# Performance work log

Hardware: AMD Instinct MI355X
Metric: run time of the kernel (lower is better)

The kernel has to match this reference:

```python
import jax, jax.numpy as jnp
import numpy as np
from jax.scipy.special import logsumexp

PAD_IDX, SOS_IDX, EOS_IDX = 0, 1, 2
NEG = -10000.0


def setup_inputs() -> dict:
    B, T, L = 64, 256, 8
    K, E, H = 128, 256, 512      # num_tags, EMBED_SIZE, HIDDEN_SIZE
    CV, WV = 128, 50000          # char / word vocab
    key = jax.random.key(0)
    ks = jax.random.split(key, 12)
    lengths = jax.random.randint(ks[0], (B,), T // 2, T + 1)
    mask = jnp.arange(T)[None, :] < lengths[:, None]          # [B,T] contiguous prefix
    wx = jnp.where(mask, jax.random.randint(ks[1], (B, T), 3, WV), 0).astype(jnp.int32)
    cx = jax.random.randint(ks[2], (B, T, L), 0, CV).astype(jnp.int32)
    y_body = jnp.where(mask, jax.random.randint(ks[3], (B, T), 3, K), PAD_IDX)
    y = jnp.concatenate([jnp.full((B, 1), SOS_IDX, jnp.int32), y_body.astype(jnp.int32)], 1)  # [B,T+1]
    s = 0.05
    char_emb = s * jax.random.normal(ks[4], (CV, E), jnp.float32)
    word_emb = s * jax.random.normal(ks[5], (WV, E), jnp.float32)
    Wi = s * jax.random.normal(ks[6], (E, 4 * H), jnp.float32)
    Wh = s * jax.random.normal(ks[7], (H, 4 * H), jnp.float32)
    b = jnp.zeros((4 * H,), jnp.float32)
    Wout = s * jax.random.normal(ks[8], (H, K), jnp.float32)
    bout = jnp.zeros((K,), jnp.float32)
    trans = jax.random.normal(ks[9], (K, K), jnp.float32)
    trans = trans.at[SOS_IDX, :].set(NEG)
    trans = trans.at[:, EOS_IDX].set(NEG)
    trans = trans.at[:, PAD_IDX].set(NEG)
    trans = trans.at[PAD_IDX, :].set(NEG)
    trans = trans.at[PAD_IDX, EOS_IDX].set(0.0)
    trans = trans.at[PAD_IDX, PAD_IDX].set(0.0)
    return dict(cx=cx, wx=wx, y=y, char_emb=char_emb, word_emb=word_emb,
                Wi=Wi, Wh=Wh, b=b, Wout=Wout, bout=bout, trans=trans)


def _forward(cx, wx, y, char_emb, word_emb, Wi, Wh, b, Wout, bout, trans):
    B, T = wx.shape
    K = trans.shape[0]
    H = Wh.shape[0]
    mask = (wx > 0)                                            # [B,T] bool
    maskf = mask.astype(jnp.float32)
    # embedding: word lookup + mean-pooled char lookup
    x = word_emb[wx] + char_emb[cx].mean(axis=2)               # [B,T,E]

    # masked LSTM (equivalent to pack_padded for prefix masks)
    def lstm_step(carry, inp):
        h, c = carry
        xt, mt = inp                                            # [B,E], [B,1]
        z = xt @ Wi + h @ Wh + b                                # [B,4H]
        i, f, g, o = jnp.split(z, 4, axis=-1)
        i, f, o = jax.nn.sigmoid(i), jax.nn.sigmoid(f), jax.nn.sigmoid(o)
        c_new = f * c + i * jnp.tanh(g)
        h_new = o * jnp.tanh(c_new)
        h = jnp.where(mt, h_new, h)
        c = jnp.where(mt, c_new, c)
        return (h, c), h

    h0 = jnp.zeros((B, H), x.dtype)
    xs = jnp.swapaxes(x, 0, 1)                                  # [T,B,E]
    ms = jnp.swapaxes(mask, 0, 1)[..., None]                    # [T,B,1]
    _, hs = jax.lax.scan(lstm_step, (h0, h0), (xs, ms))         # [T,B,H]
    hs = jnp.swapaxes(hs, 0, 1)                                 # [B,T,H]
    h = (hs @ Wout + bout) * maskf[..., None]                   # emissions [B,T,K]

    # CRF forward algorithm (log partition Z)
    score0 = jnp.full((B, K), NEG, h.dtype).at[:, SOS_IDX].set(0.0)

    def crf_step(score, inp):
        em, mt = inp                                            # [B,K], [B,1]
        s_t = logsumexp(score[:, None, :] + em[:, :, None] + trans[None, :, :], axis=-1)
        return jnp.where(mt, s_t, score), None

    emT = jnp.swapaxes(h, 0, 1)                                 # [T,B,K]
    scoreZ, _ = jax.lax.scan(crf_step, score0, (emT, ms))
    Z = logsumexp(scoreZ + trans[EOS_IDX], axis=-1)             # [B]

    # gold path score
    y_prev, y_next = y[:, :-1], y[:, 1:]                        # [B,T]
    emit = jnp.take_along_axis(h, y_next[..., None], axis=-1)[..., 0]  # [B,T]
    tr = trans[y_next, y_prev]                                  # [B,T]
    gold = jnp.sum((emit + tr) * maskf, axis=1)                 # [B]
    lengths = mask.sum(axis=1)
    last_tag = y[jnp.arange(B), lengths]                        # y has T+1 cols
    gold = gold + trans[EOS_IDX, last_tag]
    return Z - gold                                             # NLL per sequence [B]


def reference(cx, wx, y, char_emb, word_emb, Wi, Wh, b, Wout, bout, trans):
    return _forward(cx, wx, y, char_emb, word_emb, Wi, Wh, b, Wout, bout, trans)
```

## Files before the change

### kernel.cpp

```cpp
#include <hip/hip_runtime.h>


typedef float f32x4 __attribute__((ext_vector_type(4)));
typedef float f32x16 __attribute__((ext_vector_type(16)));
typedef __bf16 bf16x8 __attribute__((ext_vector_type(8)));
typedef unsigned int u32x4 __attribute__((ext_vector_type(4)));
typedef unsigned int u32x2 __attribute__((ext_vector_type(2)));

#define T_LEN 256
#define BB    64
#define EE    256
#define HH    512
#define KK    128
#define KCAT  768

static __device__ inline unsigned f2bf(float f) {
  union { float f; unsigned u; } v; v.f = f;
  unsigned r = v.u + 0x7FFF + ((v.u >> 16) & 1);
  return r >> 16;
}
static __device__ inline float sigm(float x) { return 1.f / (1.f + __expf(-x)); }
static __device__ inline float tanh_fast(float x) {
  return 1.f - 2.f / (1.f + __expf(2.f * x));
}
static __device__ inline bf16x8 ubf(u32x4 v) {
  union { u32x4 u; bf16x8 b; } c; c.u = v; return c.b;
}

__global__ __launch_bounds__(256) void build_wcat(
    const float* __restrict__ Wi, const float* __restrict__ Wh,
    unsigned short* __restrict__ WcatT) {
  __shared__ float tile[64][65];
  int ct = blockIdx.x & 31, kt = blockIdx.x >> 5;
  int tc = threadIdx.x & 63, tr = threadIdx.x >> 6;
  int c0 = ct * 64, k0 = kt * 64;
#pragma unroll
  for (int i = 0; i < 16; ++i) {
    int r = tr * 16 + i, k = k0 + r;
    float v = (k < EE) ? Wi[(size_t)k * 2048 + c0 + tc]
                       : Wh[(size_t)(k - EE) * 2048 + c0 + tc];
    tile[r][tc] = v;
  }
  __syncthreads();
#pragma unroll
  for (int i = 0; i < 16; ++i) {
    int cL = tr * 16 + i;
    WcatT[(size_t)(c0 + cL) * KCAT + k0 + tc] = (unsigned short)f2bf(tile[tc][cL]);
  }
}

__global__ __launch_bounds__(256) void build_wout(
    const float* __restrict__ Wout, unsigned short* __restrict__ WoutT) {
  __shared__ float tile[64][65];
  int ct = blockIdx.x & 1, kt = blockIdx.x >> 1;
  int tc = threadIdx.x & 63, tr = threadIdx.x >> 6;
  int c0 = ct * 64, k0 = kt * 64;
#pragma unroll
  for (int i = 0; i < 16; ++i) {
    int r = tr * 16 + i;
    tile[r][tc] = Wout[(size_t)(k0 + r) * KK + c0 + tc];
  }
  __syncthreads();
#pragma unroll
  for (int i = 0; i < 16; ++i) {
    int cL = tr * 16 + i;
    WoutT[(size_t)(c0 + cL) * HH + k0 + tc] = (unsigned short)f2bf(tile[tc][cL]);
  }
}

__global__ __launch_bounds__(256) void embed_kernel(
    const int* __restrict__ wx, const int* __restrict__ cx,
    const float* __restrict__ we, const float* __restrict__ ce,
    unsigned short* __restrict__ x) {
  int bid = blockIdx.x;
  int t = bid >> 6, b = bid & 63;
  int e = threadIdx.x;
  int w = wx[b * T_LEN + t];
  float v = we[(size_t)w * EE + e];
  const int* cp = cx + ((size_t)(b * T_LEN + t)) * 8;
  float s = 0.f;
#pragma unroll
  for (int l = 0; l < 8; ++l) s += ce[(size_t)cp[l] * EE + e];
  v += s * 0.125f;
  x[(size_t)bid * EE + e] = (unsigned short)f2bf(v);
}

__global__ void zero_flags(unsigned int* __restrict__ f) {
  unsigned z = 0u;
  asm volatile("global_store_dword %0, %1, off sc0 sc1"
               :: "v"(f + threadIdx.x), "v"(z) : "memory");
}

#define SBAR __builtin_amdgcn_sched_barrier(0)
#define WAITV(N) do { asm volatile("s_waitcnt vmcnt(" #N ")" ::: "memory"); SBAR; } while (0)
#define LDC(dst, ptr, OFF) \
  asm volatile("global_load_dwordx4 %0, %1, off offset:" OFF " sc0 sc1" \
               : "=v"(dst) : "v"(ptr) : "memory")
#define LDN(dst, ptr, OFF) \
  asm volatile("global_load_dwordx4 %0, %1, off offset:" OFF \
               : "=v"(dst) : "v"(ptr) : "memory")

#define ISSUE_X(B, P) do { \
  LDN(B[0],P,"0");   LDN(B[1],P,"32");  LDN(B[2],P,"64");  LDN(B[3],P,"96"); \
  LDN(B[4],P,"128"); LDN(B[5],P,"160"); LDN(B[6],P,"192"); LDN(B[7],P,"224"); \
  LDN(B[8],P,"256"); LDN(B[9],P,"288"); LDN(B[10],P,"320"); LDN(B[11],P,"352"); \
  LDN(B[12],P,"384"); LDN(B[13],P,"416"); LDN(B[14],P,"448"); LDN(B[15],P,"480"); } while (0)
#define ISSUE_H0(B, P) do { \
  LDC(B[0],P,"0");   LDC(B[1],P,"32");  LDC(B[2],P,"64");  LDC(B[3],P,"96"); \
  LDC(B[4],P,"128"); LDC(B[5],P,"160"); LDC(B[6],P,"192"); LDC(B[7],P,"224"); \
  LDC(B[8],P,"256"); LDC(B[9],P,"288"); LDC(B[10],P,"320"); LDC(B[11],P,"352"); \
  LDC(B[12],P,"384"); LDC(B[13],P,"416"); LDC(B[14],P,"448"); LDC(B[15],P,"480"); } while (0)
#define ISSUE_H1(B, P) do { \
  LDC(B[0],P,"512"); LDC(B[1],P,"544"); LDC(B[2],P,"576"); LDC(B[3],P,"608"); \
  LDC(B[4],P,"640"); LDC(B[5],P,"672"); LDC(B[6],P,"704"); LDC(B[7],P,"736"); \
  LDC(B[8],P,"768"); LDC(B[9],P,"800"); LDC(B[10],P,"832"); LDC(B[11],P,"864"); \
  LDC(B[12],P,"896"); LDC(B[13],P,"928"); LDC(B[14],P,"960"); LDC(B[15],P,"992"); } while (0)

#define GATES_STORE(T) do { \
    bool mk = ((int)wxv) > 0; \
    _Pragma("unroll") \
    for (int r = 0; r < 4; ++r) { \
      float zi = acc[r], zf = acc[4 + r], zg = acc[8 + r], zo = acc[12 + r]; \
      float cn = sigm(zf) * cst[r] + sigm(zi) * tanh_fast(zg); \
      float hn = sigm(zo) * tanh_fast(cn); \
      if (mk) { cst[r] = cn; hst[r] = hn; } \
    } \
    u32x2 ph; \
    ph[0] = f2bf(hst[0]) | (f2bf(hst[1]) << 16); \
    ph[1] = f2bf(hst[2]) | (f2bf(hst[3]) << 16); \
    asm volatile("global_store_dwordx2 %0, %1, off sc0 sc1" \
                 :: "v"(hstore + (size_t)(T) * 65536), "v"(ph) : "memory"); \
  } while (0)

__global__ __launch_bounds__(128, 1) void lstm_persistent(
    const unsigned short* __restrict__ x,
    unsigned short* __restrict__ hs,
    const unsigned short* __restrict__ WcatT,
    const float* __restrict__ bias,
    const int* __restrict__ wx,
    unsigned int* __restrict__ flags) {
  const int tid = threadIdx.x;
  const int lane = tid & 63;
  const int bhalf = tid >> 6;
  const int hi = lane >> 5;
  const int batch = bhalf * 32 + (lane & 31);
  const int u0 = blockIdx.x * 8;
  const int rr = lane & 31;
  const int wcol = (rr >> 3) * HH + u0 + (rr & 7);

  bf16x8 wreg[48];
#pragma unroll
  for (int kf = 0; kf < 48; ++kf)
    wreg[kf] = *(const bf16x8*)(WcatT + (size_t)wcol * KCAT + kf * 16 + hi * 8);

  float bv[16];
#pragma unroll
  for (int q = 0; q < 4; ++q)
#pragma unroll
    for (int r = 0; r < 4; ++r)
      bv[q * 4 + r] = bias[q * HH + u0 + 4 * hi + r];

  const char* xlane  = (const char*)x  + ((size_t)batch * EE + hi * 8) * 2;
  const char* hread  = (const char*)hs + ((size_t)batch * HH + hi * 8) * 2;
  char*       hstore = (char*)hs + ((size_t)batch * HH + u0 + 4 * hi) * 2;
  const int*  wxp    = wx + batch * T_LEN;

  float cst[4] = {0.f, 0.f, 0.f, 0.f};
  float hst[4] = {0.f, 0.f, 0.f, 0.f};
  u32x4 bufX[16], bufH[16];
  unsigned wxv;
  f32x16 acc;

  ISSUE_X(bufX, xlane);
  asm volatile("global_load_dword %0, %1, off" : "=v"(wxv) : "v"(wxp) : "memory");
  WAITV(0);
#pragma unroll
  for (int i = 0; i < 16; ++i) acc[i] = bv[i];
#pragma unroll
  for (int kf = 0; kf < 16; ++kf)
    acc = __builtin_amdgcn_mfma_f32_32x32x16_bf16(wreg[kf], ubf(bufX[kf]), acc, 0, 0, 0);
  GATES_STORE(0);
  WAITV(0);
  __syncthreads();
  if (tid == 0)
    __hip_atomic_store(flags + blockIdx.x, 1u, __ATOMIC_RELAXED, __HIP_MEMORY_SCOPE_AGENT);

  for (int t = 1; t < T_LEN; ++t) {
    const char* xt = xlane + (size_t)t * 32768;
    const char* hp = hread + (size_t)(t - 1) * 65536;

    ISSUE_X(bufX, xt);
    asm volatile("global_load_dword %0, %1, off" : "=v"(wxv) : "v"(wxp + t) : "memory");
    {
      unsigned v;
      do {
        asm volatile("global_load_dword %0, %1, off sc0 sc1\n\ts_waitcnt vmcnt(0)"
                     : "=v"(v) : "v"(flags + lane) : "memory");
      } while (!__all((int)(v >= (unsigned)t)));
      SBAR;
    }
    ISSUE_H0(bufH, hp);
#pragma unroll
    for (int i = 0; i < 16; ++i) acc[i] = bv[i];
#pragma unroll
    for (int kf = 0; kf < 16; ++kf)
      acc = __builtin_amdgcn_mfma_f32_32x32x16_bf16(wreg[kf], ubf(bufX[kf]), acc, 0, 0, 0);
    SBAR;
    ISSUE_H1(bufX, hp);
    WAITV(16);
#pragma unroll
    for (int kf = 0; kf < 16; ++kf)
      acc = __builtin_amdgcn_mfma_f32_32x32x16_bf16(wreg[16 + kf], ubf(bufH[kf]), acc, 0, 0, 0);
    WAITV(0);
#pragma unroll
    for (int kf = 0; kf < 16; ++kf)
      acc = __builtin_amdgcn_mfma_f32_32x32x16_bf16(wreg[32 + kf], ubf(bufX[kf]), acc, 0, 0, 0);
    GATES_STORE(t);
    WAITV(0);
    __syncthreads();
    if (tid == 0)
      __hip_atomic_store(flags + blockIdx.x, (unsigned)(t + 1),
                         __ATOMIC_RELAXED, __HIP_MEMORY_SCOPE_AGENT);
  }
}

__global__ __launch_bounds__(512) void em_gemm(
    const unsigned short* __restrict__ hs,
    const unsigned short* __restrict__ WoutT,
    const float* __restrict__ bout,
    const int* __restrict__ wx,
    float* __restrict__ em) {
  int mg = blockIdx.x;
  int wave = threadIdx.x >> 6, lane = threadIdx.x & 63;
  int m = wave >> 1, nh = wave & 1;
  int arow = lane & 15, kg = (lane >> 4) * 8;
  int rbase = mg * 64 + m * 16;
  const unsigned short* A = hs + (size_t)(rbase + arow) * HH + kg;
  f32x4 acc[4];
#pragma unroll
  for (int nt = 0; nt < 4; ++nt) acc[nt] = (f32x4){0.f, 0.f, 0.f, 0.f};
#pragma unroll
  for (int ks = 0; ks < 16; ++ks) {
    bf16x8 a = *(const bf16x8*)(A + ks * 32);
#pragma unroll
    for (int nt = 0; nt < 4; ++nt) {
      const unsigned short* Bp =
          WoutT + (size_t)(nh * 64 + nt * 16 + arow) * HH + kg + ks * 32;
      acc[nt] = __builtin_amdgcn_mfma_f32_16x16x32_bf16(a, *(const bf16x8*)Bp, acc[nt], 0, 0, 0);
    }
  }
#pragma unroll
  for (int nt = 0; nt < 4; ++nt) {
    int n = nh * 64 + nt * 16 + arow;
    float bo = bout[n];
#pragma unroll
    for (int r = 0; r < 4; ++r) {
      int row = rbase + (lane >> 4) * 4 + r;
      int t = row >> 6, b = row & 63;
      float v = (acc[nt][r] + bo) * ((wx[b * T_LEN + t] > 0) ? 1.f : 0.f);
      em[(size_t)row * KK + n] = v;
    }
  }
}

__global__ __launch_bounds__(512) void crf_kernel(
    const float* __restrict__ em,
    const float* __restrict__ trans,
    const int* __restrict__ wx,
    const int* __restrict__ y,
    float* __restrict__ out) {
  int b = blockIdx.x;
  __shared__ float tl[KK][129];
  __shared__ float El[KK][129];
  __shared__ float sc[KK];
  __shared__ float p[KK];
  __shared__ float red[512];
  __shared__ float red2[512];
  __shared__ float mshare[2];
  int tid = threadIdx.x;
  for (int i = tid; i < KK * KK; i += 512) {
    float v = trans[i];
    tl[i >> 7][i & 127] = v;
    El[i >> 7][i & 127] = __expf(v);
  }
  if (tid < KK) sc[tid] = (tid == 1) ? 0.f : -10000.f;
  __syncthreads();

  int k = tid & 127, q = tid >> 7, j0 = q * 32;
  float msc = 0.f;

  for (int t = 0; t < T_LEN; ++t) {
    if (wx[b * T_LEN + t] <= 0) continue;
    if (tid < KK) p[tid] = __expf(sc[tid] - msc);
    __syncthreads();
    float S = 0.f;
#pragma unroll
    for (int j = 0; j < 32; ++j) S += El[k][j0 + j] * p[j0 + j];
    red[tid] = S;
    __syncthreads();
    if (q == 0) {
      float Sk = S + red[128 + k] + red[256 + k] + red[384 + k];
      float ns = em[(size_t)(t * BB + b) * KK + k] + msc + __logf(Sk);
      sc[k] = ns;
      float m = ns;
#pragma unroll
      for (int off = 32; off; off >>= 1) m = fmaxf(m, __shfl_xor(m, off));
      if ((tid & 63) == 0) mshare[tid >> 6] = m;
    }
    __syncthreads();
    msc = fmaxf(mshare[0], mshare[1]);
  }

  float term = 0.f, cnt = 0.f;
  if (tid < T_LEN) {
    int yp = y[b * 257 + tid], yn = y[b * 257 + tid + 1];
    if (wx[b * T_LEN + tid] > 0) {
      term = em[(size_t)(tid * BB + b) * KK + yn] + tl[yn][yp];
      cnt = 1.f;
    }
  }
  red[tid] = term; red2[tid] = cnt;
  __syncthreads();
  for (int s2 = 256; s2 > 0; s2 >>= 1) {
    if (tid < s2) { red[tid] += red[tid + s2]; red2[tid] += red2[tid + s2]; }
    __syncthreads();
  }
  float gold = red[0];
  int len = (int)(red2[0] + 0.5f);
  __syncthreads();

  float v = (tid < KK) ? sc[tid] + tl[2][tid] : -3.0e38f;
  red[tid] = v;
  __syncthreads();
  for (int s2 = 256; s2 > 0; s2 >>= 1) {
    if (tid < s2) red[tid] = fmaxf(red[tid], red[tid + s2]);
    __syncthreads();
  }
  float mz = red[0];
  __syncthreads();
  red[tid] = (tid < KK) ? __expf(v - mz) : 0.f;
  __syncthreads();
  for (int s2 = 256; s2 > 0; s2 >>= 1) {
    if (tid < s2) red[tid] += red[tid + s2];
    __syncthreads();
  }
  if (tid == 0) {
    float Z = mz + __logf(red[0]);
    int last_tag = y[b * 257 + len];
    out[b] = Z - (gold + tl[2][last_tag]);
  }
}

extern "C" void kernel_launch(void* const* d_in, const int* in_sizes, int n_in,
                              void* d_out, int out_size, void* d_ws, size_t ws_size,
                              hipStream_t stream) {
  const int*   cx    = (const int*)d_in[0];
  const int*   wx    = (const int*)d_in[1];
  const int*   y     = (const int*)d_in[2];
  const float* ce    = (const float*)d_in[3];
  const float* we    = (const float*)d_in[4];
  const float* Wi    = (const float*)d_in[5];
  const float* Wh    = (const float*)d_in[6];
  const float* bias  = (const float*)d_in[7];
  const float* Wout  = (const float*)d_in[8];
  const float* bout  = (const float*)d_in[9];
  const float* trans = (const float*)d_in[10];
  float* out = (float*)d_out;

  char* ws = (char*)d_ws;
  unsigned short* WcatT = (unsigned short*)(ws + 0);
  unsigned short* WoutT = (unsigned short*)(ws + 3145728);
  unsigned short* x     = (unsigned short*)(ws + 3276800);
  unsigned short* hs    = (unsigned short*)(ws + 11665408);
  unsigned int*   flags = (unsigned int*)(ws + 28442624);
  float*          em    = (float*)(ws + 3276800);

  build_wcat<<<384, 256, 0, stream>>>(Wi, Wh, WcatT);
  build_wout<<<16, 256, 0, stream>>>(Wout, WoutT);
  embed_kernel<<<T_LEN * BB, 256, 0, stream>>>(wx, cx, we, ce, x);
  zero_flags<<<1, 64, 0, stream>>>(flags);
  lstm_persistent<<<64, 128, 0, stream>>>(x, hs, WcatT, bias, wx, flags);
  em_gemm<<<256, 512, 0, stream>>>(hs, WoutT, bout, wx, em);
  crf_kernel<<<BB, 512, 0, stream>>>(em, trans, wx, y, out);
}
```

Measured before the change: 1.739 ms.

## Use per-wave flags and fragment-ordered hidden-state exchange in persistent LSTM

Drops the block-wide __syncthreads and single per-block flag in the recurrent loop. Each wave now publishes its own flag, and consumers poll both flags of a block with one dwordx2 load. The hidden-state buffer is rearranged so each wave's stores and the MFMA operand loads are contiguous 1KB chunks. em_gemm is changed to stage one timestep's h tile into LDS and read it in the new layout. The spin loop gains an iteration cap that could silently break synchronization if a wait runs very long.

```diff
diff --git a/kernel.cpp b/kernel.cpp
--- a/kernel.cpp
+++ b/kernel.cpp
@@ -105,36 +105,16 @@
   LDN(B[4],P,"128"); LDN(B[5],P,"160"); LDN(B[6],P,"192"); LDN(B[7],P,"224"); \
   LDN(B[8],P,"256"); LDN(B[9],P,"288"); LDN(B[10],P,"320"); LDN(B[11],P,"352"); \
   LDN(B[12],P,"384"); LDN(B[13],P,"416"); LDN(B[14],P,"448"); LDN(B[15],P,"480"); } while (0)
-#define ISSUE_H0(B, P) do { \
-  LDC(B[0],P,"0");   LDC(B[1],P,"32");  LDC(B[2],P,"64");  LDC(B[3],P,"96"); \
-  LDC(B[4],P,"128"); LDC(B[5],P,"160"); LDC(B[6],P,"192"); LDC(B[7],P,"224"); \
-  LDC(B[8],P,"256"); LDC(B[9],P,"288"); LDC(B[10],P,"320"); LDC(B[11],P,"352"); \
-  LDC(B[12],P,"384"); LDC(B[13],P,"416"); LDC(B[14],P,"448"); LDC(B[15],P,"480"); } while (0)
-#define ISSUE_H1(B, P) do { \
-  LDC(B[0],P,"512"); LDC(B[1],P,"544"); LDC(B[2],P,"576"); LDC(B[3],P,"608"); \
-  LDC(B[4],P,"640"); LDC(B[5],P,"672"); LDC(B[6],P,"704"); LDC(B[7],P,"736"); \
-  LDC(B[8],P,"768"); LDC(B[9],P,"800"); LDC(B[10],P,"832"); LDC(B[11],P,"864"); \
-  LDC(B[12],P,"896"); LDC(B[13],P,"928"); LDC(B[14],P,"960"); LDC(B[15],P,"992"); } while (0)
-
-#define GATES_STORE(T) do { \
-    bool mk = ((int)wxv) > 0; \
-    _Pragma("unroll") \
-    for (int r = 0; r < 4; ++r) { \
-      float zi = acc[r], zf = acc[4 + r], zg = acc[8 + r], zo = acc[12 + r]; \
-      float cn = sigm(zf) * cst[r] + sigm(zi) * tanh_fast(zg); \
-      float hn = sigm(zo) * tanh_fast(cn); \
-      if (mk) { cst[r] = cn; hst[r] = hn; } \
-    } \
-    u32x2 ph; \
-    ph[0] = f2bf(hst[0]) | (f2bf(hst[1]) << 16); \
-    ph[1] = f2bf(hst[2]) | (f2bf(hst[3]) << 16); \
-    asm volatile("global_store_dwordx2 %0, %1, off sc0 sc1" \
-                 :: "v"(hstore + (size_t)(T) * 65536), "v"(ph) : "memory"); \
-  } while (0)
+
+#define ISSUE_HG(B, P0, P1, P2, P3) do { \
+  LDC(B[0],P0,"0"); LDC(B[1],P0,"1024"); LDC(B[2],P0,"2048"); LDC(B[3],P0,"3072"); \
+  LDC(B[4],P1,"0"); LDC(B[5],P1,"1024"); LDC(B[6],P1,"2048"); LDC(B[7],P1,"3072"); \
+  LDC(B[8],P2,"0"); LDC(B[9],P2,"1024"); LDC(B[10],P2,"2048"); LDC(B[11],P2,"3072"); \
+  LDC(B[12],P3,"0"); LDC(B[13],P3,"1024"); LDC(B[14],P3,"2048"); LDC(B[15],P3,"3072"); } while (0)
 
 __global__ __launch_bounds__(128, 1) void lstm_persistent(
     const unsigned short* __restrict__ x,
-    unsigned short* __restrict__ hs,
+    unsigned short* __restrict__ hxch,
     const unsigned short* __restrict__ WcatT,
     const float* __restrict__ bias,
     const int* __restrict__ wx,
@@ -144,7 +124,8 @@
   const int bhalf = tid >> 6;
   const int hi = lane >> 5;
   const int batch = bhalf * 32 + (lane & 31);
-  const int u0 = blockIdx.x * 8;
+  const int bid = blockIdx.x;
+  const int u0 = bid * 8;
   const int rr = lane & 31;
   const int wcol = (rr >> 3) * HH + u0 + (rr & 7);
 
@@ -160,10 +141,12 @@
     for (int r = 0; r < 4; ++r)
       bv[q * 4 + r] = bias[q * HH + u0 + 4 * hi + r];
 
-  const char* xlane  = (const char*)x  + ((size_t)batch * EE + hi * 8) * 2;
-  const char* hread  = (const char*)hs + ((size_t)batch * HH + hi * 8) * 2;
-  char*       hstore = (char*)hs + ((size_t)batch * HH + u0 + 4 * hi) * 2;
-  const int*  wxp    = wx + batch * T_LEN;
+  const char* xlane = (const char*)x + ((size_t)batch * EE + hi * 8) * 2;
+  const char* hread = (const char*)hxch + (size_t)bhalf * 32768 + (size_t)lane * 16;
+  char* hstore = (char*)hxch + (size_t)bhalf * 32768 + (size_t)(bid >> 1) * 1024 +
+                 ((size_t)((lane & 31) + 32 * (bid & 1))) * 16 + hi * 8;
+  const int* wxp = wx + batch * T_LEN;
+  unsigned int* myflag = flags + bid * 2 + bhalf;
 
   float cst[4] = {0.f, 0.f, 0.f, 0.f};
   float hst[4] = {0.f, 0.f, 0.f, 0.f};
@@ -179,34 +162,55 @@
 #pragma unroll
   for (int kf = 0; kf < 16; ++kf)
     acc = __builtin_amdgcn_mfma_f32_32x32x16_bf16(wreg[kf], ubf(bufX[kf]), acc, 0, 0, 0);
-  GATES_STORE(0);
+  {
+    bool mk = ((int)wxv) > 0;
+#pragma unroll
+    for (int r = 0; r < 4; ++r) {
+      float zi = acc[r], zf = acc[4 + r], zg = acc[8 + r], zo = acc[12 + r];
+      float cn = sigm(zf) * cst[r] + sigm(zi) * tanh_fast(zg);
+      float hn = sigm(zo) * tanh_fast(cn);
+      if (mk) { cst[r] = cn; hst[r] = hn; }
+    }
+    u32x2 ph;
+    ph[0] = f2bf(hst[0]) | (f2bf(hst[1]) << 16);
+    ph[1] = f2bf(hst[2]) | (f2bf(hst[3]) << 16);
+    asm volatile("global_store_dwordx2 %0, %1, off sc0 sc1"
+                 :: "v"(hstore), "v"(ph) : "memory");
+  }
   WAITV(0);
-  __syncthreads();
-  if (tid == 0)
-    __hip_atomic_store(flags + blockIdx.x, 1u, __ATOMIC_RELAXED, __HIP_MEMORY_SCOPE_AGENT);
+  __hip_atomic_store(myflag, 1u, __ATOMIC_RELAXED, __HIP_MEMORY_SCOPE_AGENT);
 
   for (int t = 1; t < T_LEN; ++t) {
     const char* xt = xlane + (size_t)t * 32768;
-    const char* hp = hread + (size_t)(t - 1) * 65536;
+    const char* hb0 = hread + (size_t)(t - 1) * 65536;
+    const char* hb1 = hb0 + 4096;
+    const char* hb2 = hb0 + 8192;
+    const char* hb3 = hb0 + 12288;
+    const char* hb4 = hb0 + 16384;
+    const char* hb5 = hb0 + 20480;
+    const char* hb6 = hb0 + 24576;
+    const char* hb7 = hb0 + 28672;
 
     ISSUE_X(bufX, xt);
     asm volatile("global_load_dword %0, %1, off" : "=v"(wxv) : "v"(wxp + t) : "memory");
     {
-      unsigned v;
-      do {
-        asm volatile("global_load_dword %0, %1, off sc0 sc1\n\ts_waitcnt vmcnt(0)"
-                     : "=v"(v) : "v"(flags + lane) : "memory");
-      } while (!__all((int)(v >= (unsigned)t)));
+      u32x2 fv; int it = 0;
+      for (;;) {
+        asm volatile("global_load_dwordx2 %0, %1, off sc0 sc1\n\ts_waitcnt vmcnt(0)"
+                     : "=v"(fv) : "v"(flags + lane * 2) : "memory");
+        if (__all((int)(fv[0] >= (unsigned)t && fv[1] >= (unsigned)t))) break;
+        if (++it >= (1 << 20)) break;
+      }
       SBAR;
     }
-    ISSUE_H0(bufH, hp);
+    ISSUE_HG(bufH, hb0, hb1, hb2, hb3);
 #pragma unroll
     for (int i = 0; i < 16; ++i) acc[i] = bv[i];
 #pragma unroll
     for (int kf = 0; kf < 16; ++kf)
       acc = __builtin_amdgcn_mfma_f32_32x32x16_bf16(wreg[kf], ubf(bufX[kf]), acc, 0, 0, 0);
     SBAR;
-    ISSUE_H1(bufX, hp);
+    ISSUE_HG(bufX, hb4, hb5, hb6, hb7);
     WAITV(16);
 #pragma unroll
     for (int kf = 0; kf < 16; ++kf)
@@ -215,37 +219,57 @@
 #pragma unroll
     for (int kf = 0; kf < 16; ++kf)
       acc = __builtin_amdgcn_mfma_f32_32x32x16_bf16(wreg[32 + kf], ubf(bufX[kf]), acc, 0, 0, 0);
-    GATES_STORE(t);
+
+    bool mk = ((int)wxv) > 0;
+#pragma unroll
+    for (int r = 0; r < 4; ++r) {
+      float zi = acc[r], zf = acc[4 + r], zg = acc[8 + r], zo = acc[12 + r];
+      float cn = sigm(zf) * cst[r] + sigm(zi) * tanh_fast(zg);
+      float hn = sigm(zo) * tanh_fast(cn);
+      if (mk) { cst[r] = cn; hst[r] = hn; }
+    }
+    u32x2 ph;
+    ph[0] = f2bf(hst[0]) | (f2bf(hst[1]) << 16);
+    ph[1] = f2bf(hst[2]) | (f2bf(hst[3]) << 16);
+    asm volatile("global_store_dwordx2 %0, %1, off sc0 sc1"
+                 :: "v"(hstore + (size_t)t * 65536), "v"(ph) : "memory");
     WAITV(0);
-    __syncthreads();
-    if (tid == 0)
-      __hip_atomic_store(flags + blockIdx.x, (unsigned)(t + 1),
-                         __ATOMIC_RELAXED, __HIP_MEMORY_SCOPE_AGENT);
+    __hip_atomic_store(myflag, (unsigned)(t + 1),
+                       __ATOMIC_RELAXED, __HIP_MEMORY_SCOPE_AGENT);
   }
 }
 
 __global__ __launch_bounds__(512) void em_gemm(
-    const unsigned short* __restrict__ hs,
+    const unsigned short* __restrict__ hxch,
     const unsigned short* __restrict__ WoutT,
     const float* __restrict__ bout,
     const int* __restrict__ wx,
     float* __restrict__ em) {
-  int mg = blockIdx.x;
-  int wave = threadIdx.x >> 6, lane = threadIdx.x & 63;
+  __shared__ unsigned short hl[32768];
+  int t = blockIdx.x;
+  int tid = threadIdx.x;
+  const char* src = (const char*)hxch + (size_t)t * 65536;
+#pragma unroll
+  for (int i = 0; i < 8; ++i)
+    *(u32x4*)(&hl[(size_t)(i * 512 + tid) * 8]) =
+        *(const u32x4*)(src + (size_t)(i * 512 + tid) * 16);
+  __syncthreads();
+
+  int wave = tid >> 6, lane = tid & 63;
   int m = wave >> 1, nh = wave & 1;
-  int arow = lane & 15, kg = (lane >> 4) * 8;
-  int rbase = mg * 64 + m * 16;
-  const unsigned short* A = hs + (size_t)(rbase + arow) * HH + kg;
+  int arow = lane & 15, l4 = lane >> 4;
+  int b = m * 16 + arow;
+  int cb = (b >> 5) * 2048 + (b & 31) + 32 * (l4 & 1) + (l4 >> 1) * 64;
   f32x4 acc[4];
 #pragma unroll
   for (int nt = 0; nt < 4; ++nt) acc[nt] = (f32x4){0.f, 0.f, 0.f, 0.f};
 #pragma unroll
   for (int ks = 0; ks < 16; ++ks) {
-    bf16x8 a = *(const bf16x8*)(A + ks * 32);
+    bf16x8 a = *(const bf16x8*)(&hl[(size_t)(cb + ks * 128) * 8]);
 #pragma unroll
     for (int nt = 0; nt < 4; ++nt) {
       const unsigned short* Bp =
-          WoutT + (size_t)(nh * 64 + nt * 16 + arow) * HH + kg + ks * 32;
+          WoutT + (size_t)(nh * 64 + nt * 16 + arow) * HH + l4 * 8 + ks * 32;
       acc[nt] = __builtin_amdgcn_mfma_f32_16x16x32_bf16(a, *(const bf16x8*)Bp, acc[nt], 0, 0, 0);
     }
   }
@@ -255,9 +279,9 @@
     float bo = bout[n];
 #pragma unroll
     for (int r = 0; r < 4; ++r) {
-      int row = rbase + (lane >> 4) * 4 + r;
-      int t = row >> 6, b = row & 63;
-      float v = (acc[nt][r] + bo) * ((wx[b * T_LEN + t] > 0) ? 1.f : 0.f);
+      int row = t * 64 + m * 16 + l4 * 4 + r;
+      int bb = row & 63;
+      float v = (acc[nt][r] + bo) * ((wx[bb * T_LEN + t] > 0) ? 1.f : 0.f);
       em[(size_t)row * KK + n] = v;
     }
   }
@@ -371,15 +395,15 @@
   unsigned short* WcatT = (unsigned short*)(ws + 0);
   unsigned short* WoutT = (unsigned short*)(ws + 3145728);
   unsigned short* x     = (unsigned short*)(ws + 3276800);
-  unsigned short* hs    = (unsigned short*)(ws + 11665408);
+  unsigned short* hxch  = (unsigned short*)(ws + 11665408);
   unsigned int*   flags = (unsigned int*)(ws + 28442624);
   float*          em    = (float*)(ws + 3276800);
 
   build_wcat<<<384, 256, 0, stream>>>(Wi, Wh, WcatT);
   build_wout<<<16, 256, 0, stream>>>(Wout, WoutT);
   embed_kernel<<<T_LEN * BB, 256, 0, stream>>>(wx, cx, we, ce, x);
-  zero_flags<<<1, 64, 0, stream>>>(flags);
-  lstm_persistent<<<64, 128, 0, stream>>>(x, hs, WcatT, bias, wx, flags);
-  em_gemm<<<256, 512, 0, stream>>>(hs, WoutT, bout, wx, em);
+  zero_flags<<<1, 128, 0, stream>>>(flags);
+  lstm_persistent<<<64, 128, 0, stream>>>(x, hxch, WcatT, bias, wx, flags);
+  em_gemm<<<256, 512, 0, stream>>>(hxch, WoutT, bout, wx, em);
   crf_kernel<<<BB, 512, 0, stream>>>(em, trans, wx, y, out);
 }
```

New measurement: 1.783 ms. +2.5%, slower.
